# Optimization experiments

Hardware: AMD Instinct MI355X
Metric: run time of the kernel (lower is better)

## Reference

```python
import jax, jax.numpy as jnp
import numpy as np

NQ = 8           # n_qubits_q
NL = 4           # n_layers_q_circuit
NW = NQ + 1      # device wires = n_qubits + 1
DIM = 768        # input_dim == output_dim
BATCH = 4096
EPS = 1e-5

CNOT = jnp.array([[1, 0, 0, 0],
                  [0, 1, 0, 0],
                  [0, 0, 0, 1],
                  [0, 0, 1, 0]], dtype=jnp.complex64).reshape(2, 2, 2, 2)


def rx_mat(t):
    c = jnp.cos(t / 2).astype(jnp.complex64)
    s = (-1j) * jnp.sin(t / 2).astype(jnp.complex64)
    return jnp.stack([jnp.stack([c, s]), jnp.stack([s, c])])


def ry_mat(t):
    c = jnp.cos(t / 2).astype(jnp.complex64)
    s = jnp.sin(t / 2).astype(jnp.complex64)
    return jnp.stack([jnp.stack([c, -s]), jnp.stack([s, c])])


def rz_mat(t):
    e = jnp.exp(-0.5j * t.astype(jnp.complex64))
    z = jnp.zeros_like(e)
    return jnp.stack([jnp.stack([e, z]), jnp.stack([z, jnp.conj(e)])])


def apply1(state, U, w):
    # state: (2,)*NW tensor; contract gate onto wire w
    st = jnp.tensordot(U, state, axes=((1,), (w,)))
    return jnp.moveaxis(st, 0, w)


def apply2(state, G, c, t):
    # G: (2,2,2,2) gate acting on (control, target)
    st = jnp.tensordot(G, state, axes=((2, 3), (c, t)))
    return jnp.moveaxis(st, (0, 1), (c, t))


def circuit(inp, w):
    # inp: [NQ] encoded angles, w: [NL, NQ+1] circuit weights
    state = jnp.zeros((2,) * NW, jnp.complex64).at[(0,) * NW].set(1.0)
    for i in range(NQ):
        state = apply1(state, rx_mat(inp[i]), i)
        state = apply1(state, rz_mat(inp[i]), i)
    for i in range(NQ):
        state = apply1(state, rx_mat(w[0, i]), i)
        state = apply1(state, rz_mat(w[1, i]), i)
    for l in range(1, NL):
        for i in range(NQ):
            state = apply2(state, CNOT, i, (i + 1) % NQ)
            state = apply1(state, ry_mat(w[l, i]), i)
            state = apply1(state, rz_mat(w[l, i]), i)
        state = apply2(state, CNOT, NQ - 1, NQ)
        state = apply1(state, ry_mat(w[l, NQ]), NQ)
    probs = jnp.abs(state) ** 2
    z = []
    for i in range(NQ):
        other = tuple(a for a in range(NW) if a != i)
        p = probs.sum(other)          # [2]
        z.append(p[0] - p[1])         # <Z_i>
    return jnp.stack(z)               # [NQ]


def setup_inputs() -> dict:
    key = jax.random.key(0)
    ks = jax.random.split(key, 6)
    x = jax.random.normal(ks[0], (BATCH, DIM), jnp.float32)
    w_in = jax.random.normal(ks[1], (NQ, DIM), jnp.float32) * np.float32(1.0 / np.sqrt(DIM))
    b_in = jnp.zeros((NQ,), jnp.float32)
    gamma = jnp.ones((NQ,), jnp.float32)
    beta = jnp.zeros((NQ,), jnp.float32)
    q_w = jax.random.uniform(ks[2], (NL, NQ + 1), jnp.float32, 0.0, 2.0 * np.pi)
    w_out = jax.random.normal(ks[3], (DIM, NQ), jnp.float32) * np.float32(1.0 / np.sqrt(NQ))
    b_out = jnp.zeros((DIM,), jnp.float32)
    return {"x": x, "w_in": w_in, "b_in": b_in, "gamma": gamma, "beta": beta,
            "q_w": q_w, "w_out": w_out, "b_out": b_out}


def reference(x, w_in, b_in, gamma, beta, q_w, w_out, b_out):
    h = jnp.tanh(x @ w_in.T + b_in)                 # input_proj + tanh, [B, NQ]
    mu = h.mean(-1, keepdims=True)
    var = ((h - mu) ** 2).mean(-1, keepdims=True)
    hn = (h - mu) / jnp.sqrt(var + EPS) * gamma + beta   # LayerNorm
    hn = jax.lax.stop_gradient(hn)                  # torch .detach() before quantum
    qz = jax.vmap(circuit, in_axes=(0, None))(hn, q_w)   # [B, NQ] expvals
    out = qz @ w_out.T + b_out                      # output_proj
    return x + out                                   # residual (input_dim == output_dim)
```

## Files before the change

### kernel.cpp

```cpp
#include <hip/hip_runtime.h>
#include <math.h>

#define DIM   768
#define BATCH 4096
#define NQ    8
#define EPSLN 1e-5f


__device__ __forceinline__ float shflx(float v, int m) { return __shfl_xor(v, m, 64); }

template<int W>
__device__ __forceinline__ void gate_rz(float (&re)[8], float (&im)[8],
                                        float c, float s, int lane) {
  if constexpr (W < 3) {
#pragma unroll
    for (int r = 0; r < 8; ++r) {
      const float t = ((r >> W) & 1) ? s : -s;
      const float xx = re[r], yy = im[r];
      re[r] = xx * c - yy * t;
      im[r] = yy * c + xx * t;
    }
  } else {
    const float t = ((lane >> (W - 3)) & 1) ? s : -s;
#pragma unroll
    for (int r = 0; r < 8; ++r) {
      const float xx = re[r], yy = im[r];
      re[r] = xx * c - yy * t;
      im[r] = yy * c + xx * t;
    }
  }
}

template<int W>
__device__ __forceinline__ void gate_rx(float (&re)[8], float (&im)[8],
                                        float c, float s) {
  if constexpr (W < 3) {
#pragma unroll
    for (int r = 0; r < 8; ++r) {
      if (!((r >> W) & 1)) {
        const int r2 = r | (1 << W);
        const float ar = re[r], ai = im[r], br = re[r2], bi = im[r2];
        re[r]  = c * ar + s * bi;
        im[r]  = c * ai - s * br;
        re[r2] = c * br + s * ai;
        im[r2] = c * bi - s * ar;
      }
    }
  } else {
    const int mask = 1 << (W - 3);
#pragma unroll
    for (int r = 0; r < 8; ++r) {
      const float ore = shflx(re[r], mask);
      const float oim = shflx(im[r], mask);
      const float xx = re[r], yy = im[r];
      re[r] = c * xx + s * oim;
      im[r] = c * yy - s * ore;
    }
  }
}

template<int W>
__device__ __forceinline__ void gate_ry(float (&re)[8], float (&im)[8],
                                        float c, float s, int lane) {
  if constexpr (W < 3) {
#pragma unroll
    for (int r = 0; r < 8; ++r) {
      if (!((r >> W) & 1)) {
        const int r2 = r | (1 << W);
        const float ar = re[r], ai = im[r], br = re[r2], bi = im[r2];
        re[r]  = c * ar - s * br;
        im[r]  = c * ai - s * bi;
        re[r2] = s * ar + c * br;
        im[r2] = s * ai + c * bi;
      }
    }
  } else {
    const int mask = 1 << (W - 3);
    const float t = ((lane >> (W - 3)) & 1) ? s : -s;
#pragma unroll
    for (int r = 0; r < 8; ++r) {
      const float ore = shflx(re[r], mask);
      const float oim = shflx(im[r], mask);
      re[r] = c * re[r] + t * ore;
      im[r] = c * im[r] + t * oim;
    }
  }
}

template<int C, int T>
__device__ __forceinline__ void gate_cnot(float (&re)[8], float (&im)[8], int lane) {
  if constexpr (C < 3 && T < 3) {
#pragma unroll
    for (int r = 0; r < 8; ++r) {
      if (((r >> C) & 1) && !((r >> T) & 1)) {
        const int r2 = r | (1 << T);
        const float tr = re[r], ti = im[r];
        re[r] = re[r2]; im[r] = im[r2];
        re[r2] = tr;    im[r2] = ti;
      }
    }
  } else if constexpr (C < 3) {
    const int mask = 1 << (T - 3);
#pragma unroll
    for (int r = 0; r < 8; ++r) {
      if ((r >> C) & 1) {
        re[r] = shflx(re[r], mask);
        im[r] = shflx(im[r], mask);
      }
    }
  } else if constexpr (T < 3) {
    const bool cc = (lane >> (C - 3)) & 1;
#pragma unroll
    for (int r = 0; r < 8; ++r) {
      if (!((r >> T) & 1)) {
        const int r2 = r | (1 << T);
        const float ar = re[r], ai = im[r], br = re[r2], bi = im[r2];
        re[r]  = cc ? br : ar;  im[r]  = cc ? bi : ai;
        re[r2] = cc ? ar : br;  im[r2] = cc ? ai : bi;
      }
    }
  } else {
    const int mask = 1 << (T - 3);
    const bool cc = (lane >> (C - 3)) & 1;
#pragma unroll
    for (int r = 0; r < 8; ++r) {
      const float ore = shflx(re[r], mask);
      const float oim = shflx(im[r], mask);
      re[r] = cc ? ore : re[r];
      im[r] = cc ? oim : im[r];
    }
  }
}

__global__ void precompute_trig(const float* __restrict__ qw, float* __restrict__ cs) {
  const int i = threadIdx.x;
  if (i < 36) {
    float s, c;
    sincosf(0.5f * qw[i], &s, &c);
    cs[2 * i]     = c;
    cs[2 * i + 1] = s;
  }
}

__global__ __launch_bounds__(256, 4)
void quantum_fused(const float* __restrict__ x,
                   const float* __restrict__ w_in,
                   const float* __restrict__ b_in,
                   const float* __restrict__ gamma,
                   const float* __restrict__ beta,
                   const float* __restrict__ w_out,
                   const float* __restrict__ b_out,
                   const float* __restrict__ cs,
                   float* __restrict__ out) {
  const int lane = threadIdx.x & 63;
  const int wv   = threadIdx.x >> 6;
  const int row  = blockIdx.x * 4 + wv;

  const float* xrow = x + (size_t)row * DIM;
  const float4* xv  = (const float4*)xrow;

  float4 xr[3];
#pragma unroll
  for (int k = 0; k < 3; ++k) xr[k] = xv[lane + 64 * k];

  float h[8];
#pragma unroll
  for (int q = 0; q < 8; ++q) {
    const float4* wq = (const float4*)(w_in + q * DIM);
    float acc = 0.f;
#pragma unroll
    for (int k = 0; k < 3; ++k) {
      const float4 w4 = wq[lane + 64 * k];
      acc += xr[k].x * w4.x + xr[k].y * w4.y + xr[k].z * w4.z + xr[k].w * w4.w;
    }
    h[q] = acc;
  }
#pragma unroll
  for (int m = 1; m < 64; m <<= 1) {
#pragma unroll
    for (int q = 0; q < 8; ++q) h[q] += shflx(h[q], m);
  }

#pragma unroll
  for (int q = 0; q < 8; ++q) h[q] = tanhf(h[q] + b_in[q]);
  float mu = 0.f;
#pragma unroll
  for (int q = 0; q < 8; ++q) mu += h[q];
  mu *= 0.125f;
  float var = 0.f;
#pragma unroll
  for (int q = 0; q < 8; ++q) { const float d = h[q] - mu; var += d * d; }
  var *= 0.125f;
  const float inv = 1.0f / sqrtf(var + EPSLN);
  float ang[8];
#pragma unroll
  for (int q = 0; q < 8; ++q)
    ang[q] = (h[q] - mu) * inv * gamma[q] + beta[q];

  float re[8], im[8];
#pragma unroll
  for (int r = 0; r < 8; ++r) { re[r] = 0.f; im[r] = 0.f; }
  re[0] = (lane == 0) ? 1.f : 0.f;

#define ENC_I(i) { float s_, c_; sincosf(0.5f * ang[i], &s_, &c_);            \
                   gate_rx<i>(re, im, c_, s_);                                 \
                   gate_rz<i>(re, im, c_, s_, lane); }
  ENC_I(0) ENC_I(1) ENC_I(2) ENC_I(3) ENC_I(4) ENC_I(5) ENC_I(6) ENC_I(7)
#undef ENC_I

#define L0_I(i) { gate_rx<i>(re, im, cs[2*(i)], cs[2*(i)+1]);                  \
                  gate_rz<i>(re, im, cs[2*(9+(i))], cs[2*(9+(i))+1], lane); }
  L0_I(0) L0_I(1) L0_I(2) L0_I(3) L0_I(4) L0_I(5) L0_I(6) L0_I(7)
#undef L0_I

#define LSTEP(l, i, j) { gate_cnot<i, j>(re, im, lane);                        \
                         const float c_ = cs[2*((l)*9+(i))];                   \
                         const float s_ = cs[2*((l)*9+(i))+1];                 \
                         gate_ry<i>(re, im, c_, s_, lane);                     \
                         gate_rz<i>(re, im, c_, s_, lane); }
#define LAYER(l)                                                               \
  LSTEP(l,0,1) LSTEP(l,1,2) LSTEP(l,2,3) LSTEP(l,3,4)                          \
  LSTEP(l,4,5) LSTEP(l,5,6) LSTEP(l,6,7) LSTEP(l,7,0)                          \
  { gate_cnot<7, 8>(re, im, lane);                                             \
    gate_ry<8>(re, im, cs[2*((l)*9+8)], cs[2*((l)*9+8)+1], lane); }
  LAYER(1) LAYER(2) LAYER(3)
#undef LAYER
#undef LSTEP

  float p[8];
#pragma unroll
  for (int r = 0; r < 8; ++r) p[r] = re[r] * re[r] + im[r] * im[r];
  float ptot = 0.f;
#pragma unroll
  for (int r = 0; r < 8; ++r) ptot += p[r];
  float z[8];
#pragma unroll
  for (int i = 0; i < 3; ++i) {
    float acc = 0.f;
#pragma unroll
    for (int r = 0; r < 8; ++r) acc += ((r >> i) & 1) ? -p[r] : p[r];
    z[i] = acc;
  }
#pragma unroll
  for (int i = 3; i < 8; ++i)
    z[i] = ((lane >> (i - 3)) & 1) ? -ptot : ptot;
#pragma unroll
  for (int m = 1; m < 64; m <<= 1) {
#pragma unroll
    for (int i = 0; i < 8; ++i) z[i] += shflx(z[i], m);
  }

  float* orow = out + (size_t)row * DIM;
  float4* ov = (float4*)orow;
  const float4* bv = (const float4*)b_out;
#pragma unroll
  for (int k = 0; k < 3; ++k) {
    const int j4 = lane + 64 * k;
    const float4 b4 = bv[j4];
    const float4* wo = (const float4*)(w_out + (size_t)j4 * 32);
    const float4 r0a = wo[0], r0b = wo[1];
    const float4 r1a = wo[2], r1b = wo[3];
    const float4 r2a = wo[4], r2b = wo[5];
    const float4 r3a = wo[6], r3b = wo[7];
    float4 o;
    o.x = xr[k].x + b4.x + z[0]*r0a.x + z[1]*r0a.y + z[2]*r0a.z + z[3]*r0a.w
                        + z[4]*r0b.x + z[5]*r0b.y + z[6]*r0b.z + z[7]*r0b.w;
    o.y = xr[k].y + b4.y + z[0]*r1a.x + z[1]*r1a.y + z[2]*r1a.z + z[3]*r1a.w
                        + z[4]*r1b.x + z[5]*r1b.y + z[6]*r1b.z + z[7]*r1b.w;
    o.z = xr[k].z + b4.z + z[0]*r2a.x + z[1]*r2a.y + z[2]*r2a.z + z[3]*r2a.w
                        + z[4]*r2b.x + z[5]*r2b.y + z[6]*r2b.z + z[7]*r2b.w;
    o.w = xr[k].w + b4.w + z[0]*r3a.x + z[1]*r3a.y + z[2]*r3a.z + z[3]*r3a.w
                        + z[4]*r3b.x + z[5]*r3b.y + z[6]*r3b.z + z[7]*r3b.w;
    ov[j4] = o;
  }
}

extern "C" void kernel_launch(void* const* d_in, const int* in_sizes, int n_in,
                              void* d_out, int out_size, void* d_ws, size_t ws_size,
                              hipStream_t stream) {
  const float* x     = (const float*)d_in[0];
  const float* w_in  = (const float*)d_in[1];
  const float* b_in  = (const float*)d_in[2];
  const float* gamma = (const float*)d_in[3];
  const float* beta  = (const float*)d_in[4];
  const float* q_w   = (const float*)d_in[5];
  const float* w_out = (const float*)d_in[6];
  const float* b_out = (const float*)d_in[7];
  float* outp = (float*)d_out;
  float* cs   = (float*)d_ws;

  hipLaunchKernelGGL(precompute_trig, dim3(1), dim3(64), 0, stream, q_w, cs);
  hipLaunchKernelGGL(quantum_fused, dim3(BATCH / 4), dim3(256), 0, stream,
                     x, w_in, b_in, gamma, beta, w_out, b_out, cs, outp);
}
```

Measured before the change: 118.4 us.

## Process two batch rows per wavefront to amortize weight loads and shuffles

Each wavefront now simulates two circuits at once, holding 16 complex amplitudes per lane, and the grid shrinks to BATCH/8 blocks. The w_in, w_out and gate-parameter loads and the per-gate control logic are shared between the two rows, and batching the shuffles into arrays gives more instruction-level parallelism to hide cross-lane latency. In exchange, register pressure roughly doubles (launch bounds lowered to 2 waves) and fewer waves are resident to hide memory latency.

```diff
diff --git a/kernel.cpp b/kernel.cpp
--- a/kernel.cpp
+++ b/kernel.cpp
@@ -10,20 +10,25 @@
 __device__ __forceinline__ float shflx(float v, int m) { return __shfl_xor(v, m, 64); }
 
 template<int W>
-__device__ __forceinline__ void gate_rz(float (&re)[8], float (&im)[8],
-                                        float c, float s, int lane) {
+__device__ __forceinline__ void gate_rz(float (&re)[16], float (&im)[16],
+                                        float c0, float s0, float c1, float s1,
+                                        int lane) {
   if constexpr (W < 3) {
 #pragma unroll
-    for (int r = 0; r < 8; ++r) {
-      const float t = ((r >> W) & 1) ? s : -s;
+    for (int r = 0; r < 16; ++r) {
+      const float c = (r < 8) ? c0 : c1;
+      const float t = (((r >> W) & 1) ? 1.f : -1.f) * ((r < 8) ? s0 : s1);
       const float xx = re[r], yy = im[r];
       re[r] = xx * c - yy * t;
       im[r] = yy * c + xx * t;
     }
   } else {
-    const float t = ((lane >> (W - 3)) & 1) ? s : -s;
-#pragma unroll
-    for (int r = 0; r < 8; ++r) {
+    const float sgn = ((lane >> (W - 3)) & 1) ? 1.f : -1.f;
+    const float t0 = sgn * s0, t1 = sgn * s1;
+#pragma unroll
+    for (int r = 0; r < 16; ++r) {
+      const float c = (r < 8) ? c0 : c1;
+      const float t = (r < 8) ? t0 : t1;
       const float xx = re[r], yy = im[r];
       re[r] = xx * c - yy * t;
       im[r] = yy * c + xx * t;
@@ -32,13 +37,15 @@
 }
 
 template<int W>
-__device__ __forceinline__ void gate_rx(float (&re)[8], float (&im)[8],
-                                        float c, float s) {
+__device__ __forceinline__ void gate_rx(float (&re)[16], float (&im)[16],
+                                        float c0, float s0, float c1, float s1) {
   if constexpr (W < 3) {
 #pragma unroll
-    for (int r = 0; r < 8; ++r) {
+    for (int r = 0; r < 16; ++r) {
       if (!((r >> W) & 1)) {
         const int r2 = r | (1 << W);
+        const float c = (r < 8) ? c0 : c1;
+        const float s = (r < 8) ? s0 : s1;
         const float ar = re[r], ai = im[r], br = re[r2], bi = im[r2];
         re[r]  = c * ar + s * bi;
         im[r]  = c * ai - s * br;
@@ -48,25 +55,31 @@
     }
   } else {
     const int mask = 1 << (W - 3);
-#pragma unroll
-    for (int r = 0; r < 8; ++r) {
-      const float ore = shflx(re[r], mask);
-      const float oim = shflx(im[r], mask);
+    float ore[16], oim[16];
+#pragma unroll
+    for (int r = 0; r < 16; ++r) { ore[r] = shflx(re[r], mask); oim[r] = shflx(im[r], mask); }
+#pragma unroll
+    for (int r = 0; r < 16; ++r) {
+      const float c = (r < 8) ? c0 : c1;
+      const float s = (r < 8) ? s0 : s1;
       const float xx = re[r], yy = im[r];
-      re[r] = c * xx + s * oim;
-      im[r] = c * yy - s * ore;
+      re[r] = c * xx + s * oim[r];
+      im[r] = c * yy - s * ore[r];
     }
   }
 }
 
 template<int W>
-__device__ __forceinline__ void gate_ry(float (&re)[8], float (&im)[8],
-                                        float c, float s, int lane) {
+__device__ __forceinline__ void gate_ry(float (&re)[16], float (&im)[16],
+                                        float c0, float s0, float c1, float s1,
+                                        int lane) {
   if constexpr (W < 3) {
 #pragma unroll
-    for (int r = 0; r < 8; ++r) {
+    for (int r = 0; r < 16; ++r) {
       if (!((r >> W) & 1)) {
         const int r2 = r | (1 << W);
+        const float c = (r < 8) ? c0 : c1;
+        const float s = (r < 8) ? s0 : s1;
         const float ar = re[r], ai = im[r], br = re[r2], bi = im[r2];
         re[r]  = c * ar - s * br;
         im[r]  = c * ai - s * bi;
@@ -76,22 +89,26 @@
     }
   } else {
     const int mask = 1 << (W - 3);
-    const float t = ((lane >> (W - 3)) & 1) ? s : -s;
-#pragma unroll
-    for (int r = 0; r < 8; ++r) {
-      const float ore = shflx(re[r], mask);
-      const float oim = shflx(im[r], mask);
-      re[r] = c * re[r] + t * ore;
-      im[r] = c * im[r] + t * oim;
+    const float sgn = ((lane >> (W - 3)) & 1) ? 1.f : -1.f;
+    const float t0 = sgn * s0, t1 = sgn * s1;
+    float ore[16], oim[16];
+#pragma unroll
+    for (int r = 0; r < 16; ++r) { ore[r] = shflx(re[r], mask); oim[r] = shflx(im[r], mask); }
+#pragma unroll
+    for (int r = 0; r < 16; ++r) {
+      const float c = (r < 8) ? c0 : c1;
+      const float t = (r < 8) ? t0 : t1;
+      re[r] = c * re[r] + t * ore[r];
+      im[r] = c * im[r] + t * oim[r];
     }
   }
 }
 
 template<int C, int T>
-__device__ __forceinline__ void gate_cnot(float (&re)[8], float (&im)[8], int lane) {
+__device__ __forceinline__ void gate_cnot(float (&re)[16], float (&im)[16], int lane) {
   if constexpr (C < 3 && T < 3) {
 #pragma unroll
-    for (int r = 0; r < 8; ++r) {
+    for (int r = 0; r < 16; ++r) {
       if (((r >> C) & 1) && !((r >> T) & 1)) {
         const int r2 = r | (1 << T);
         const float tr = re[r], ti = im[r];
@@ -102,7 +119,7 @@
   } else if constexpr (C < 3) {
     const int mask = 1 << (T - 3);
 #pragma unroll
-    for (int r = 0; r < 8; ++r) {
+    for (int r = 0; r < 16; ++r) {
       if ((r >> C) & 1) {
         re[r] = shflx(re[r], mask);
         im[r] = shflx(im[r], mask);
@@ -111,7 +128,7 @@
   } else if constexpr (T < 3) {
     const bool cc = (lane >> (C - 3)) & 1;
 #pragma unroll
-    for (int r = 0; r < 8; ++r) {
+    for (int r = 0; r < 16; ++r) {
       if (!((r >> T) & 1)) {
         const int r2 = r | (1 << T);
         const float ar = re[r], ai = im[r], br = re[r2], bi = im[r2];
@@ -122,12 +139,13 @@
   } else {
     const int mask = 1 << (T - 3);
     const bool cc = (lane >> (C - 3)) & 1;
-#pragma unroll
-    for (int r = 0; r < 8; ++r) {
-      const float ore = shflx(re[r], mask);
-      const float oim = shflx(im[r], mask);
-      re[r] = cc ? ore : re[r];
-      im[r] = cc ? oim : im[r];
+    float ore[16], oim[16];
+#pragma unroll
+    for (int r = 0; r < 16; ++r) { ore[r] = shflx(re[r], mask); oim[r] = shflx(im[r], mask); }
+#pragma unroll
+    for (int r = 0; r < 16; ++r) {
+      re[r] = cc ? ore[r] : re[r];
+      im[r] = cc ? oim[r] : im[r];
     }
   }
 }
@@ -142,7 +160,7 @@
   }
 }
 
-__global__ __launch_bounds__(256, 4)
+__global__ __launch_bounds__(256, 2)
 void quantum_fused(const float* __restrict__ x,
                    const float* __restrict__ w_in,
                    const float* __restrict__ b_in,
@@ -154,124 +172,148 @@
                    float* __restrict__ out) {
   const int lane = threadIdx.x & 63;
   const int wv   = threadIdx.x >> 6;
-  const int row  = blockIdx.x * 4 + wv;
-
-  const float* xrow = x + (size_t)row * DIM;
-  const float4* xv  = (const float4*)xrow;
-
-  float4 xr[3];
-#pragma unroll
-  for (int k = 0; k < 3; ++k) xr[k] = xv[lane + 64 * k];
-
-  float h[8];
+  const int rowA = blockIdx.x * 8 + wv * 2;
+  const int rowB = rowA + 1;
+
+  const float4* xvA = (const float4*)(x + (size_t)rowA * DIM);
+  const float4* xvB = (const float4*)(x + (size_t)rowB * DIM);
+
+  float4 xrA[3], xrB[3];
+#pragma unroll
+  for (int k = 0; k < 3; ++k) { xrA[k] = xvA[lane + 64 * k]; xrB[k] = xvB[lane + 64 * k]; }
+
+  float h[16];
 #pragma unroll
   for (int q = 0; q < 8; ++q) {
     const float4* wq = (const float4*)(w_in + q * DIM);
-    float acc = 0.f;
+    float aA = 0.f, aB = 0.f;
 #pragma unroll
     for (int k = 0; k < 3; ++k) {
       const float4 w4 = wq[lane + 64 * k];
-      acc += xr[k].x * w4.x + xr[k].y * w4.y + xr[k].z * w4.z + xr[k].w * w4.w;
-    }
-    h[q] = acc;
+      aA += xrA[k].x * w4.x + xrA[k].y * w4.y + xrA[k].z * w4.z + xrA[k].w * w4.w;
+      aB += xrB[k].x * w4.x + xrB[k].y * w4.y + xrB[k].z * w4.z + xrB[k].w * w4.w;
+    }
+    h[q] = aA; h[8 + q] = aB;
   }
 #pragma unroll
   for (int m = 1; m < 64; m <<= 1) {
 #pragma unroll
-    for (int q = 0; q < 8; ++q) h[q] += shflx(h[q], m);
-  }
-
-#pragma unroll
-  for (int q = 0; q < 8; ++q) h[q] = tanhf(h[q] + b_in[q]);
-  float mu = 0.f;
-#pragma unroll
-  for (int q = 0; q < 8; ++q) mu += h[q];
-  mu *= 0.125f;
-  float var = 0.f;
-#pragma unroll
-  for (int q = 0; q < 8; ++q) { const float d = h[q] - mu; var += d * d; }
-  var *= 0.125f;
-  const float inv = 1.0f / sqrtf(var + EPSLN);
-  float ang[8];
-#pragma unroll
-  for (int q = 0; q < 8; ++q)
-    ang[q] = (h[q] - mu) * inv * gamma[q] + beta[q];
-
-  float re[8], im[8];
-#pragma unroll
-  for (int r = 0; r < 8; ++r) { re[r] = 0.f; im[r] = 0.f; }
+    for (int q = 0; q < 16; ++q) h[q] += shflx(h[q], m);
+  }
+
+  float ang[16];
+#pragma unroll
+  for (int rowi = 0; rowi < 2; ++rowi) {
+    const int o = rowi * 8;
+#pragma unroll
+    for (int q = 0; q < 8; ++q) h[o + q] = tanhf(h[o + q] + b_in[q]);
+    float mu = 0.f;
+#pragma unroll
+    for (int q = 0; q < 8; ++q) mu += h[o + q];
+    mu *= 0.125f;
+    float var = 0.f;
+#pragma unroll
+    for (int q = 0; q < 8; ++q) { const float d = h[o + q] - mu; var += d * d; }
+    var *= 0.125f;
+    const float inv = 1.0f / sqrtf(var + EPSLN);
+#pragma unroll
+    for (int q = 0; q < 8; ++q)
+      ang[o + q] = (h[o + q] - mu) * inv * gamma[q] + beta[q];
+  }
+
+  float re[16], im[16];
+#pragma unroll
+  for (int r = 0; r < 16; ++r) { re[r] = 0.f; im[r] = 0.f; }
   re[0] = (lane == 0) ? 1.f : 0.f;
-
-#define ENC_I(i) { float s_, c_; sincosf(0.5f * ang[i], &s_, &c_);            \
-                   gate_rx<i>(re, im, c_, s_);                                 \
-                   gate_rz<i>(re, im, c_, s_, lane); }
+  re[8] = (lane == 0) ? 1.f : 0.f;
+
+#define ENC_I(i) { float sA, cA, sB, cB;                                       \
+                   sincosf(0.5f * ang[i], &sA, &cA);                           \
+                   sincosf(0.5f * ang[8 + i], &sB, &cB);                       \
+                   gate_rx<i>(re, im, cA, sA, cB, sB);                         \
+                   gate_rz<i>(re, im, cA, sA, cB, sB, lane); }
   ENC_I(0) ENC_I(1) ENC_I(2) ENC_I(3) ENC_I(4) ENC_I(5) ENC_I(6) ENC_I(7)
 #undef ENC_I
 
-#define L0_I(i) { gate_rx<i>(re, im, cs[2*(i)], cs[2*(i)+1]);                  \
-                  gate_rz<i>(re, im, cs[2*(9+(i))], cs[2*(9+(i))+1], lane); }
+#define L0_I(i) { const float c0 = cs[2*(i)],     s0 = cs[2*(i)+1];            \
+                  const float c1 = cs[2*(9+(i))], s1 = cs[2*(9+(i))+1];        \
+                  gate_rx<i>(re, im, c0, s0, c0, s0);                          \
+                  gate_rz<i>(re, im, c1, s1, c1, s1, lane); }
   L0_I(0) L0_I(1) L0_I(2) L0_I(3) L0_I(4) L0_I(5) L0_I(6) L0_I(7)
 #undef L0_I
 
 #define LSTEP(l, i, j) { gate_cnot<i, j>(re, im, lane);                        \
                          const float c_ = cs[2*((l)*9+(i))];                   \
                          const float s_ = cs[2*((l)*9+(i))+1];                 \
-                         gate_ry<i>(re, im, c_, s_, lane);                     \
-                         gate_rz<i>(re, im, c_, s_, lane); }
+                         gate_ry<i>(re, im, c_, s_, c_, s_, lane);             \
+                         gate_rz<i>(re, im, c_, s_, c_, s_, lane); }
 #define LAYER(l)                                                               \
   LSTEP(l,0,1) LSTEP(l,1,2) LSTEP(l,2,3) LSTEP(l,3,4)                          \
   LSTEP(l,4,5) LSTEP(l,5,6) LSTEP(l,6,7) LSTEP(l,7,0)                          \
   { gate_cnot<7, 8>(re, im, lane);                                             \
-    gate_ry<8>(re, im, cs[2*((l)*9+8)], cs[2*((l)*9+8)+1], lane); }
+    gate_ry<8>(re, im, cs[2*((l)*9+8)], cs[2*((l)*9+8)+1],                     \
+                        cs[2*((l)*9+8)], cs[2*((l)*9+8)+1], lane); }
   LAYER(1) LAYER(2) LAYER(3)
 #undef LAYER
 #undef LSTEP
 
-  float p[8];
-#pragma unroll
-  for (int r = 0; r < 8; ++r) p[r] = re[r] * re[r] + im[r] * im[r];
-  float ptot = 0.f;
-#pragma unroll
-  for (int r = 0; r < 8; ++r) ptot += p[r];
-  float z[8];
+  float p[16];
+#pragma unroll
+  for (int r = 0; r < 16; ++r) p[r] = re[r] * re[r] + im[r] * im[r];
+  float ptotA = 0.f, ptotB = 0.f;
+#pragma unroll
+  for (int r = 0; r < 8; ++r) { ptotA += p[r]; ptotB += p[8 + r]; }
+  float z[16];
 #pragma unroll
   for (int i = 0; i < 3; ++i) {
-    float acc = 0.f;
-#pragma unroll
-    for (int r = 0; r < 8; ++r) acc += ((r >> i) & 1) ? -p[r] : p[r];
-    z[i] = acc;
-  }
-#pragma unroll
-  for (int i = 3; i < 8; ++i)
-    z[i] = ((lane >> (i - 3)) & 1) ? -ptot : ptot;
+    float aA = 0.f, aB = 0.f;
+#pragma unroll
+    for (int r = 0; r < 8; ++r) {
+      const float sg = ((r >> i) & 1) ? -1.f : 1.f;
+      aA += sg * p[r];
+      aB += sg * p[8 + r];
+    }
+    z[i] = aA; z[8 + i] = aB;
+  }
+#pragma unroll
+  for (int i = 3; i < 8; ++i) {
+    const float sg = ((lane >> (i - 3)) & 1) ? -1.f : 1.f;
+    z[i] = sg * ptotA;
+    z[8 + i] = sg * ptotB;
+  }
 #pragma unroll
   for (int m = 1; m < 64; m <<= 1) {
 #pragma unroll
-    for (int i = 0; i < 8; ++i) z[i] += shflx(z[i], m);
-  }
-
-  float* orow = out + (size_t)row * DIM;
-  float4* ov = (float4*)orow;
-  const float4* bv = (const float4*)b_out;
-#pragma unroll
-  for (int k = 0; k < 3; ++k) {
-    const int j4 = lane + 64 * k;
-    const float4 b4 = bv[j4];
-    const float4* wo = (const float4*)(w_out + (size_t)j4 * 32);
-    const float4 r0a = wo[0], r0b = wo[1];
-    const float4 r1a = wo[2], r1b = wo[3];
-    const float4 r2a = wo[4], r2b = wo[5];
-    const float4 r3a = wo[6], r3b = wo[7];
-    float4 o;
-    o.x = xr[k].x + b4.x + z[0]*r0a.x + z[1]*r0a.y + z[2]*r0a.z + z[3]*r0a.w
-                        + z[4]*r0b.x + z[5]*r0b.y + z[6]*r0b.z + z[7]*r0b.w;
-    o.y = xr[k].y + b4.y + z[0]*r1a.x + z[1]*r1a.y + z[2]*r1a.z + z[3]*r1a.w
-                        + z[4]*r1b.x + z[5]*r1b.y + z[6]*r1b.z + z[7]*r1b.w;
-    o.z = xr[k].z + b4.z + z[0]*r2a.x + z[1]*r2a.y + z[2]*r2a.z + z[3]*r2a.w
-                        + z[4]*r2b.x + z[5]*r2b.y + z[6]*r2b.z + z[7]*r2b.w;
-    o.w = xr[k].w + b4.w + z[0]*r3a.x + z[1]*r3a.y + z[2]*r3a.z + z[3]*r3a.w
-                        + z[4]*r3b.x + z[5]*r3b.y + z[6]*r3b.z + z[7]*r3b.w;
-    ov[j4] = o;
+    for (int i = 0; i < 16; ++i) z[i] += shflx(z[i], m);
+  }
+
+#pragma unroll
+  for (int rowi = 0; rowi < 2; ++rowi) {
+    const int row = rowi ? rowB : rowA;
+    const float4* xr = rowi ? xrB : xrA;
+    const float* zz = z + rowi * 8;
+    float4* ov = (float4*)(out + (size_t)row * DIM);
+    const float4* bv = (const float4*)b_out;
+#pragma unroll
+    for (int k = 0; k < 3; ++k) {
+      const int j4 = lane + 64 * k;
+      const float4 b4 = bv[j4];
+      const float4* wo = (const float4*)(w_out + (size_t)j4 * 32);
+      const float4 r0a = wo[0], r0b = wo[1];
+      const float4 r1a = wo[2], r1b = wo[3];
+      const float4 r2a = wo[4], r2b = wo[5];
+      const float4 r3a = wo[6], r3b = wo[7];
+      float4 o;
+      o.x = xr[k].x + b4.x + zz[0]*r0a.x + zz[1]*r0a.y + zz[2]*r0a.z + zz[3]*r0a.w
+                          + zz[4]*r0b.x + zz[5]*r0b.y + zz[6]*r0b.z + zz[7]*r0b.w;
+      o.y = xr[k].y + b4.y + zz[0]*r1a.x + zz[1]*r1a.y + zz[2]*r1a.z + zz[3]*r1a.w
+                          + zz[4]*r1b.x + zz[5]*r1b.y + zz[6]*r1b.z + zz[7]*r1b.w;
+      o.z = xr[k].z + b4.z + zz[0]*r2a.x + zz[1]*r2a.y + zz[2]*r2a.z + zz[3]*r2a.w
+                          + zz[4]*r2b.x + zz[5]*r2b.y + zz[6]*r2b.z + zz[7]*r2b.w;
+      o.w = xr[k].w + b4.w + zz[0]*r3a.x + zz[1]*r3a.y + zz[2]*r3a.z + zz[3]*r3a.w
+                          + zz[4]*r3b.x + zz[5]*r3b.y + zz[6]*r3b.z + zz[7]*r3b.w;
+      ov[j4] = o;
+    }
   }
 }
 
@@ -290,6 +332,6 @@
   float* cs   = (float*)d_ws;
 
   hipLaunchKernelGGL(precompute_trig, dim3(1), dim3(64), 0, stream, q_w, cs);
-  hipLaunchKernelGGL(quantum_fused, dim3(BATCH / 4), dim3(256), 0, stream,
+  hipLaunchKernelGGL(quantum_fused, dim3(BATCH / 8), dim3(256), 0, stream,
                      x, w_in, b_in, gamma, beta, w_out, b_out, cs, outp);
 }
```

Result: slower. 127.7 us (+7.8%).

## Build product-state analytically, remap qubit lanes, use DPP/swizzle cross-lane ops

Applied to the files above, without the earlier changes.

The encoding and first-layer rotations act on separate qubits, so the state after them is a product state. It is now built directly as a tensor product of per-qubit 2-vectors instead of applying 32 gates with shuffles. Qubit-to-lane-bit assignments are permuted so the most frequent cross-lane partners map to cheap DPP or ds_swizzle patterns, and permlane32_swap is used for xor 32 where the builtin exists. Reductions use the same fast cross-lane primitives. The risks are the faster __sincosf losing precision and errors in the bit mapping.

```diff
diff --git a/kernel.cpp b/kernel.cpp
--- a/kernel.cpp
+++ b/kernel.cpp
@@ -3,11 +3,58 @@
 
 #define DIM   768
 #define BATCH 4096
-#define NQ    8
 #define EPSLN 1e-5f
 
 
-__device__ __forceinline__ float shflx(float v, int m) { return __shfl_xor(v, m, 64); }
+__host__ __device__ constexpr int bitof(int W) {
+  return W == 3 ? 4 : W == 4 ? 0 : W == 5 ? 1 : W == 6 ? 3 : W == 7 ? 5 : 2;
+}
+
+template<int CTRL>
+__device__ __forceinline__ float dppf(float v) {
+  return __int_as_float(__builtin_amdgcn_update_dpp(
+      0, __float_as_int(v), CTRL, 0xF, 0xF, false));
+}
+template<int OFF>
+__device__ __forceinline__ float swzf(float v) {
+  return __int_as_float(__builtin_amdgcn_ds_swizzle(__float_as_int(v), OFF));
+}
+__device__ __forceinline__ float xor32f(float v, int lane) {
+#if __has_builtin(__builtin_amdgcn_permlane32_swap)
+  typedef int i2_t __attribute__((ext_vector_type(2)));
+  i2_t r = __builtin_amdgcn_permlane32_swap(__float_as_int(v), __float_as_int(v),
+                                            false, false);
+  return __int_as_float((lane >= 32) ? r.x : r.y);
+#else
+  return __shfl_xor(v, 32, 64);
+#endif
+}
+
+template<int M>
+__device__ __forceinline__ float lxor(float v, int lane) {
+  if constexpr (M == 1)       return dppf<0xB1>(v);
+  else if constexpr (M == 2)  return dppf<0x4E>(v);
+  else if constexpr (M == 4)  return swzf<0x101F>(v);
+  else if constexpr (M == 8)  return dppf<0x128>(v);
+  else if constexpr (M == 16) return swzf<0x401F>(v);
+  else                        return xor32f(v, lane);
+}
+
+template<int N>
+__device__ __forceinline__ void allred(float (&v)[N], int lane) {
+#pragma unroll
+  for (int q = 0; q < N; ++q) v[q] += lxor<1>(v[q], lane);
+#pragma unroll
+  for (int q = 0; q < N; ++q) v[q] += lxor<2>(v[q], lane);
+#pragma unroll
+  for (int q = 0; q < N; ++q) v[q] += lxor<4>(v[q], lane);
+#pragma unroll
+  for (int q = 0; q < N; ++q) v[q] += lxor<8>(v[q], lane);
+#pragma unroll
+  for (int q = 0; q < N; ++q) v[q] += lxor<16>(v[q], lane);
+#pragma unroll
+  for (int q = 0; q < N; ++q) v[q] += lxor<32>(v[q], lane);
+}
 
 template<int W>
 __device__ __forceinline__ void gate_rz(float (&re)[8], float (&im)[8],
@@ -21,40 +68,12 @@
       im[r] = yy * c + xx * t;
     }
   } else {
-    const float t = ((lane >> (W - 3)) & 1) ? s : -s;
+    const float t = ((lane >> bitof(W)) & 1) ? s : -s;
 #pragma unroll
     for (int r = 0; r < 8; ++r) {
       const float xx = re[r], yy = im[r];
       re[r] = xx * c - yy * t;
       im[r] = yy * c + xx * t;
-    }
-  }
-}
-
-template<int W>
-__device__ __forceinline__ void gate_rx(float (&re)[8], float (&im)[8],
-                                        float c, float s) {
-  if constexpr (W < 3) {
-#pragma unroll
-    for (int r = 0; r < 8; ++r) {
-      if (!((r >> W) & 1)) {
-        const int r2 = r | (1 << W);
-        const float ar = re[r], ai = im[r], br = re[r2], bi = im[r2];
-        re[r]  = c * ar + s * bi;
-        im[r]  = c * ai - s * br;
-        re[r2] = c * br + s * ai;
-        im[r2] = c * bi - s * ar;
-      }
-    }
-  } else {
-    const int mask = 1 << (W - 3);
-#pragma unroll
-    for (int r = 0; r < 8; ++r) {
-      const float ore = shflx(re[r], mask);
-      const float oim = shflx(im[r], mask);
-      const float xx = re[r], yy = im[r];
-      re[r] = c * xx + s * oim;
-      im[r] = c * yy - s * ore;
     }
   }
 }
@@ -75,12 +94,12 @@
       }
     }
   } else {
-    const int mask = 1 << (W - 3);
-    const float t = ((lane >> (W - 3)) & 1) ? s : -s;
-#pragma unroll
-    for (int r = 0; r < 8; ++r) {
-      const float ore = shflx(re[r], mask);
-      const float oim = shflx(im[r], mask);
+    constexpr int M = 1 << bitof(W);
+    const float t = ((lane >> bitof(W)) & 1) ? s : -s;
+#pragma unroll
+    for (int r = 0; r < 8; ++r) {
+      const float ore = lxor<M>(re[r], lane);
+      const float oim = lxor<M>(im[r], lane);
       re[r] = c * re[r] + t * ore;
       im[r] = c * im[r] + t * oim;
     }
@@ -100,16 +119,16 @@
       }
     }
   } else if constexpr (C < 3) {
-    const int mask = 1 << (T - 3);
+    constexpr int M = 1 << bitof(T);
 #pragma unroll
     for (int r = 0; r < 8; ++r) {
       if ((r >> C) & 1) {
-        re[r] = shflx(re[r], mask);
-        im[r] = shflx(im[r], mask);
+        re[r] = lxor<M>(re[r], lane);
+        im[r] = lxor<M>(im[r], lane);
       }
     }
   } else if constexpr (T < 3) {
-    const bool cc = (lane >> (C - 3)) & 1;
+    const bool cc = (lane >> bitof(C)) & 1;
 #pragma unroll
     for (int r = 0; r < 8; ++r) {
       if (!((r >> T) & 1)) {
@@ -120,16 +139,23 @@
       }
     }
   } else {
-    const int mask = 1 << (T - 3);
-    const bool cc = (lane >> (C - 3)) & 1;
-#pragma unroll
-    for (int r = 0; r < 8; ++r) {
-      const float ore = shflx(re[r], mask);
-      const float oim = shflx(im[r], mask);
-      re[r] = cc ? ore : re[r];
-      im[r] = cc ? oim : im[r];
-    }
-  }
+    constexpr int M = 1 << bitof(T);
+    const bool cc = (lane >> bitof(C)) & 1;
+#pragma unroll
+    for (int r = 0; r < 8; ++r) {
+      const float orr = lxor<M>(re[r], lane);
+      const float oii = lxor<M>(im[r], lane);
+      re[r] = cc ? orr : re[r];
+      im[r] = cc ? oii : im[r];
+    }
+  }
+}
+
+__device__ __forceinline__ void cmul(float& dr, float& di,
+                                     float ar, float ai, float br, float bi) {
+  const float rr = ar * br - ai * bi;
+  const float ii = ar * bi + ai * br;
+  dr = rr; di = ii;
 }
 
 __global__ void precompute_trig(const float* __restrict__ qw, float* __restrict__ cs) {
@@ -156,9 +182,7 @@
   const int wv   = threadIdx.x >> 6;
   const int row  = blockIdx.x * 4 + wv;
 
-  const float* xrow = x + (size_t)row * DIM;
-  const float4* xv  = (const float4*)xrow;
-
+  const float4* xv = (const float4*)(x + (size_t)row * DIM);
   float4 xr[3];
 #pragma unroll
   for (int k = 0; k < 3; ++k) xr[k] = xv[lane + 64 * k];
@@ -175,11 +199,7 @@
     }
     h[q] = acc;
   }
-#pragma unroll
-  for (int m = 1; m < 64; m <<= 1) {
-#pragma unroll
-    for (int q = 0; q < 8; ++q) h[q] += shflx(h[q], m);
-  }
+  allred(h, lane);
 
 #pragma unroll
   for (int q = 0; q < 8; ++q) h[q] = tanhf(h[q] + b_in[q]);
@@ -197,21 +217,56 @@
   for (int q = 0; q < 8; ++q)
     ang[q] = (h[q] - mu) * inv * gamma[q] + beta[q];
 
+  float f0r[8], f0i[8], f1r[8], f1i[8];
+#pragma unroll
+  for (int i = 0; i < 8; ++i) {
+    float sa, ca;
+    __sincosf(0.5f * ang[i], &sa, &ca);
+    const float p0r = ca * ca, p0i = -ca * sa;
+    const float p1r = sa * sa, p1i = -sa * ca;
+    const float c0 = cs[2 * i],        s0 = cs[2 * i + 1];
+    const float cz = cs[2 * (9 + i)],  sz = cs[2 * (9 + i) + 1];
+    const float q0r = c0 * p0r + s0 * p1i, q0i = c0 * p0i - s0 * p1r;
+    const float q1r = s0 * p0i + c0 * p1r, q1i = -s0 * p0r + c0 * p1i;
+    f0r[i] = cz * q0r + sz * q0i;  f0i[i] = cz * q0i - sz * q0r;
+    f1r[i] = cz * q1r - sz * q1i;  f1i[i] = cz * q1i + sz * q1r;
+  }
+
+  float tr[8], ti[8];
+  tr[0] = f0r[0]; ti[0] = f0i[0];
+  tr[1] = f1r[0]; ti[1] = f1i[0];
+#pragma unroll
+  for (int b = 0; b < 2; ++b) {
+    cmul(tr[2 + b], ti[2 + b], tr[b], ti[b], f1r[1], f1i[1]);
+    cmul(tr[b],     ti[b],     tr[b], ti[b], f0r[1], f0i[1]);
+  }
+#pragma unroll
+  for (int b = 0; b < 4; ++b) {
+    cmul(tr[4 + b], ti[4 + b], tr[b], ti[b], f1r[2], f1i[2]);
+    cmul(tr[b],     ti[b],     tr[b], ti[b], f0r[2], f0i[2]);
+  }
+
+  float Lr, Li;
+  {
+    const bool b3 = (lane >> bitof(3)) & 1;
+    Lr = b3 ? f1r[3] : f0r[3];
+    Li = b3 ? f1i[3] : f0i[3];
+#pragma unroll
+    for (int i = 4; i < 8; ++i) {
+      const bool b = (lane >> bitof(i)) & 1;
+      const float gr = b ? f1r[i] : f0r[i];
+      const float gi = b ? f1i[i] : f0i[i];
+      cmul(Lr, Li, Lr, Li, gr, gi);
+    }
+    if ((lane >> bitof(8)) & 1) { Lr = 0.f; Li = 0.f; }
+  }
+
   float re[8], im[8];
 #pragma unroll
-  for (int r = 0; r < 8; ++r) { re[r] = 0.f; im[r] = 0.f; }
-  re[0] = (lane == 0) ? 1.f : 0.f;
-
-#define ENC_I(i) { float s_, c_; sincosf(0.5f * ang[i], &s_, &c_);            \
-                   gate_rx<i>(re, im, c_, s_);                                 \
-                   gate_rz<i>(re, im, c_, s_, lane); }
-  ENC_I(0) ENC_I(1) ENC_I(2) ENC_I(3) ENC_I(4) ENC_I(5) ENC_I(6) ENC_I(7)
-#undef ENC_I
-
-#define L0_I(i) { gate_rx<i>(re, im, cs[2*(i)], cs[2*(i)+1]);                  \
-                  gate_rz<i>(re, im, cs[2*(9+(i))], cs[2*(9+(i))+1], lane); }
-  L0_I(0) L0_I(1) L0_I(2) L0_I(3) L0_I(4) L0_I(5) L0_I(6) L0_I(7)
-#undef L0_I
+  for (int r = 0; r < 8; ++r) {
+    re[r] = tr[r] * Lr - ti[r] * Li;
+    im[r] = tr[r] * Li + ti[r] * Lr;
+  }
 
 #define LSTEP(l, i, j) { gate_cnot<i, j>(re, im, lane);                        \
                          const float c_ = cs[2*((l)*9+(i))];                   \
@@ -243,12 +298,8 @@
   }
 #pragma unroll
   for (int i = 3; i < 8; ++i)
-    z[i] = ((lane >> (i - 3)) & 1) ? -ptot : ptot;
-#pragma unroll
-  for (int m = 1; m < 64; m <<= 1) {
-#pragma unroll
-    for (int i = 0; i < 8; ++i) z[i] += shflx(z[i], m);
-  }
+    z[i] = ((lane >> bitof(i)) & 1) ? -ptot : ptot;
+  allred(z, lane);
 
   float* orow = out + (size_t)row * DIM;
   float4* ov = (float4*)orow;
```

Result: faster. 106.0 us (-10.5%).

## Analytic product-state encoding, qubit-to-lane remap, DPP shuffles and packed FMA

Applied to the files above, without the earlier changes.

Replaces the gate-by-gate encoding and first layer with an analytic product-state construction, since before any CNOT each qubit evolves independently. Qubits are remapped onto register and lane bits so most cross-lane exchanges can use DPP or ds_swizzle instead of generic shuffles. The complex state is stored as float2 so packed FMA can be used. The per-qubit Z reductions are replaced by a Walsh-Hadamard butterfly followed by readlane. These changes target ALU and cross-lane exchange cost, at the price of more intricate bit-mapping logic where an error would give wrong results.

```diff
diff --git a/kernel.cpp b/kernel.cpp
--- a/kernel.cpp
+++ b/kernel.cpp
@@ -3,133 +3,151 @@
 
 #define DIM   768
 #define BATCH 4096
-#define NQ    8
 #define EPSLN 1e-5f
 
 
-__device__ __forceinline__ float shflx(float v, int m) { return __shfl_xor(v, m, 64); }
-
+typedef float v2f __attribute__((ext_vector_type(2)));
+
+__device__ __forceinline__ v2f pkfma(v2f a, v2f b, v2f c) {
+  return __builtin_elementwise_fma(a, b, c);
+}
+
+template<int CTRL>
+__device__ __forceinline__ float dppf(float v) {
+  return __int_as_float(__builtin_amdgcn_update_dpp(
+      0, __float_as_int(v), CTRL, 0xF, 0xF, false));
+}
+template<int OFF>
+__device__ __forceinline__ float swzf(float v) {
+  return __int_as_float(__builtin_amdgcn_ds_swizzle(__float_as_int(v), OFF));
+}
+
+template<int M>
+__device__ __forceinline__ float lxor(float v, int bpx) {
+  if constexpr (M == 1)       return dppf<0xB1>(v);
+  else if constexpr (M == 2)  return dppf<0x4E>(v);
+  else if constexpr (M == 4)  return swzf<0x101F>(v);
+  else if constexpr (M == 8)  return dppf<0x128>(v);
+  else if constexpr (M == 16) return swzf<0x401F>(v);
+  else return __int_as_float(__builtin_amdgcn_ds_bpermute(bpx, __float_as_int(v)));
+}
+template<int M>
+__device__ __forceinline__ v2f lxor2(v2f v, int bpx) {
+  v2f r; r.x = lxor<M>(v.x, bpx); r.y = lxor<M>(v.y, bpx); return r;
+}
+
+__host__ __device__ constexpr int wbit(int w) {
+  return w == 2 ? 2 : w == 3 ? 0 : w == 4 ? 1 : w == 5 ? 3 : w == 6 ? 4 : 5;
+}
+__host__ __device__ constexpr int wmask(int w) { return 1 << wbit(w); }
+
+__device__ __forceinline__ float rdlane(float v, int l) {
+  return __int_as_float(__builtin_amdgcn_readlane(__float_as_int(v), l));
+}
+__device__ __forceinline__ float rdfirst(float v) {
+  return __int_as_float(__builtin_amdgcn_readfirstlane(__float_as_int(v)));
+}
+
+__device__ __forceinline__ v2f cmul(v2f a, v2f b) {
+  v2f r;
+  r.x = fmaf(a.x, b.x, -(a.y * b.y));
+  r.y = fmaf(a.x, b.y,   a.y * b.x);
+  return r;
+}
+
+template<int B>
+__device__ __forceinline__ void rz_local(v2f (&a)[8], float c, float s) {
+  const v2f cc = {c, c};
+  const v2f t1 = {-s, s};
+  const v2f t0 = {s, -s};
+#pragma unroll
+  for (int r = 0; r < 8; ++r) {
+    const v2f tt = ((r >> B) & 1) ? t1 : t0;
+    v2f sw; sw.x = a[r].y; sw.y = a[r].x;
+    a[r] = pkfma(tt, sw, cc * a[r]);
+  }
+}
 template<int W>
-__device__ __forceinline__ void gate_rz(float (&re)[8], float (&im)[8],
-                                        float c, float s, int lane) {
-  if constexpr (W < 3) {
-#pragma unroll
-    for (int r = 0; r < 8; ++r) {
-      const float t = ((r >> W) & 1) ? s : -s;
-      const float xx = re[r], yy = im[r];
-      re[r] = xx * c - yy * t;
-      im[r] = yy * c + xx * t;
+__device__ __forceinline__ void rz_lane(v2f (&a)[8], float c, float s, bool bit) {
+  const float t = bit ? s : -s;
+  const v2f cc = {c, c}, tv = {-t, t};
+#pragma unroll
+  for (int r = 0; r < 8; ++r) {
+    v2f sw; sw.x = a[r].y; sw.y = a[r].x;
+    a[r] = pkfma(tv, sw, cc * a[r]);
+  }
+}
+template<int B>
+__device__ __forceinline__ void ry_local(v2f (&a)[8], float c, float s) {
+  const v2f cc = {c, c}, sv = {s, s}, ns = {-s, -s};
+#pragma unroll
+  for (int r = 0; r < 8; ++r) {
+    if (!((r >> B) & 1)) {
+      const int r2 = r | (1 << B);
+      const v2f lo = a[r], hi = a[r2];
+      a[r]  = pkfma(ns, hi, cc * lo);
+      a[r2] = pkfma(sv, lo, cc * hi);
     }
-  } else {
-    const float t = ((lane >> (W - 3)) & 1) ? s : -s;
-#pragma unroll
-    for (int r = 0; r < 8; ++r) {
-      const float xx = re[r], yy = im[r];
-      re[r] = xx * c - yy * t;
-      im[r] = yy * c + xx * t;
+  }
+}
+template<int W>
+__device__ __forceinline__ void ry_lane(v2f (&a)[8], float c, float s, bool bit, int bpx) {
+  constexpr int M = wmask(W);
+  const float t = bit ? s : -s;
+  const v2f cc = {c, c}, tv = {t, t};
+#pragma unroll
+  for (int r = 0; r < 8; ++r) {
+    const v2f o = lxor2<M>(a[r], bpx);
+    a[r] = pkfma(tv, o, cc * a[r]);
+  }
+}
+__device__ __forceinline__ void cnot01(v2f (&a)[8]) {
+  v2f t = a[1]; a[1] = a[3]; a[3] = t;
+  t = a[5]; a[5] = a[7]; a[7] = t;
+}
+__device__ __forceinline__ void cnot12(v2f (&a)[8], int bpx) {
+  a[2] = lxor2<4>(a[2], bpx);
+  a[3] = lxor2<4>(a[3], bpx);
+  a[6] = lxor2<4>(a[6], bpx);
+  a[7] = lxor2<4>(a[7], bpx);
+}
+template<int T>
+__device__ __forceinline__ void cnot_ll(v2f (&a)[8], bool cc, int bpx) {
+  constexpr int M = wmask(T);
+#pragma unroll
+  for (int r = 0; r < 8; ++r) {
+    const v2f o = lxor2<M>(a[r], bpx);
+    a[r].x = cc ? o.x : a[r].x;
+    a[r].y = cc ? o.y : a[r].y;
+  }
+}
+template<int B>
+__device__ __forceinline__ void cnot_lt(v2f (&a)[8], bool cc) {
+#pragma unroll
+  for (int r = 0; r < 8; ++r) {
+    if (!((r >> B) & 1)) {
+      const int r2 = r | (1 << B);
+      const v2f lo = a[r], hi = a[r2];
+      a[r].x  = cc ? hi.x : lo.x;  a[r].y  = cc ? hi.y : lo.y;
+      a[r2].x = cc ? lo.x : hi.x;  a[r2].y = cc ? lo.y : hi.y;
     }
   }
 }
 
-template<int W>
-__device__ __forceinline__ void gate_rx(float (&re)[8], float (&im)[8],
-                                        float c, float s) {
-  if constexpr (W < 3) {
-#pragma unroll
-    for (int r = 0; r < 8; ++r) {
-      if (!((r >> W) & 1)) {
-        const int r2 = r | (1 << W);
-        const float ar = re[r], ai = im[r], br = re[r2], bi = im[r2];
-        re[r]  = c * ar + s * bi;
-        im[r]  = c * ai - s * br;
-        re[r2] = c * br + s * ai;
-        im[r2] = c * bi - s * ar;
-      }
-    }
-  } else {
-    const int mask = 1 << (W - 3);
-#pragma unroll
-    for (int r = 0; r < 8; ++r) {
-      const float ore = shflx(re[r], mask);
-      const float oim = shflx(im[r], mask);
-      const float xx = re[r], yy = im[r];
-      re[r] = c * xx + s * oim;
-      im[r] = c * yy - s * ore;
-    }
-  }
-}
-
-template<int W>
-__device__ __forceinline__ void gate_ry(float (&re)[8], float (&im)[8],
-                                        float c, float s, int lane) {
-  if constexpr (W < 3) {
-#pragma unroll
-    for (int r = 0; r < 8; ++r) {
-      if (!((r >> W) & 1)) {
-        const int r2 = r | (1 << W);
-        const float ar = re[r], ai = im[r], br = re[r2], bi = im[r2];
-        re[r]  = c * ar - s * br;
-        im[r]  = c * ai - s * bi;
-        re[r2] = s * ar + c * br;
-        im[r2] = s * ai + c * bi;
-      }
-    }
-  } else {
-    const int mask = 1 << (W - 3);
-    const float t = ((lane >> (W - 3)) & 1) ? s : -s;
-#pragma unroll
-    for (int r = 0; r < 8; ++r) {
-      const float ore = shflx(re[r], mask);
-      const float oim = shflx(im[r], mask);
-      re[r] = c * re[r] + t * ore;
-      im[r] = c * im[r] + t * oim;
-    }
-  }
-}
-
-template<int C, int T>
-__device__ __forceinline__ void gate_cnot(float (&re)[8], float (&im)[8], int lane) {
-  if constexpr (C < 3 && T < 3) {
-#pragma unroll
-    for (int r = 0; r < 8; ++r) {
-      if (((r >> C) & 1) && !((r >> T) & 1)) {
-        const int r2 = r | (1 << T);
-        const float tr = re[r], ti = im[r];
-        re[r] = re[r2]; im[r] = im[r2];
-        re[r2] = tr;    im[r2] = ti;
-      }
-    }
-  } else if constexpr (C < 3) {
-    const int mask = 1 << (T - 3);
-#pragma unroll
-    for (int r = 0; r < 8; ++r) {
-      if ((r >> C) & 1) {
-        re[r] = shflx(re[r], mask);
-        im[r] = shflx(im[r], mask);
-      }
-    }
-  } else if constexpr (T < 3) {
-    const bool cc = (lane >> (C - 3)) & 1;
-#pragma unroll
-    for (int r = 0; r < 8; ++r) {
-      if (!((r >> T) & 1)) {
-        const int r2 = r | (1 << T);
-        const float ar = re[r], ai = im[r], br = re[r2], bi = im[r2];
-        re[r]  = cc ? br : ar;  im[r]  = cc ? bi : ai;
-        re[r2] = cc ? ar : br;  im[r2] = cc ? ai : bi;
-      }
-    }
-  } else {
-    const int mask = 1 << (T - 3);
-    const bool cc = (lane >> (C - 3)) & 1;
-#pragma unroll
-    for (int r = 0; r < 8; ++r) {
-      const float ore = shflx(re[r], mask);
-      const float oim = shflx(im[r], mask);
-      re[r] = cc ? ore : re[r];
-      im[r] = cc ? oim : im[r];
-    }
-  }
+template<int N>
+__device__ __forceinline__ void allred(float (&v)[N], int bpx) {
+#pragma unroll
+  for (int q = 0; q < N; ++q) v[q] += lxor<1>(v[q], bpx);
+#pragma unroll
+  for (int q = 0; q < N; ++q) v[q] += lxor<2>(v[q], bpx);
+#pragma unroll
+  for (int q = 0; q < N; ++q) v[q] += lxor<4>(v[q], bpx);
+#pragma unroll
+  for (int q = 0; q < N; ++q) v[q] += lxor<8>(v[q], bpx);
+#pragma unroll
+  for (int q = 0; q < N; ++q) v[q] += lxor<16>(v[q], bpx);
+#pragma unroll
+  for (int q = 0; q < N; ++q) v[q] += lxor<32>(v[q], bpx);
 }
 
 __global__ void precompute_trig(const float* __restrict__ qw, float* __restrict__ cs) {
@@ -155,10 +173,16 @@
   const int lane = threadIdx.x & 63;
   const int wv   = threadIdx.x >> 6;
   const int row  = blockIdx.x * 4 + wv;
-
-  const float* xrow = x + (size_t)row * DIM;
-  const float4* xv  = (const float4*)xrow;
-
+  const int bpx  = ((lane ^ 32) << 2);
+
+  const bool bw2 = (lane >> 2) & 1;
+  const bool bw3 = (lane >> 0) & 1;
+  const bool bw4 = (lane >> 1) & 1;
+  const bool bw5 = (lane >> 3) & 1;
+  const bool bw6 = (lane >> 4) & 1;
+  const bool bw7 = (lane >> 5) & 1;
+
+  const float4* xv = (const float4*)(x + (size_t)row * DIM);
   float4 xr[3];
 #pragma unroll
   for (int k = 0; k < 3; ++k) xr[k] = xv[lane + 64 * k];
@@ -167,19 +191,20 @@
 #pragma unroll
   for (int q = 0; q < 8; ++q) {
     const float4* wq = (const float4*)(w_in + q * DIM);
-    float acc = 0.f;
+    v2f acc = {0.f, 0.f};
 #pragma unroll
     for (int k = 0; k < 3; ++k) {
       const float4 w4 = wq[lane + 64 * k];
-      acc += xr[k].x * w4.x + xr[k].y * w4.y + xr[k].z * w4.z + xr[k].w * w4.w;
+      v2f xa; xa.x = xr[k].x; xa.y = xr[k].y;
+      v2f xb; xb.x = xr[k].z; xb.y = xr[k].w;
+      v2f wa; wa.x = w4.x; wa.y = w4.y;
+      v2f wb; wb.x = w4.z; wb.y = w4.w;
+      acc = pkfma(xa, wa, acc);
+      acc = pkfma(xb, wb, acc);
     }
-    h[q] = acc;
-  }
-#pragma unroll
-  for (int m = 1; m < 64; m <<= 1) {
-#pragma unroll
-    for (int q = 0; q < 8; ++q) h[q] += shflx(h[q], m);
-  }
+    h[q] = acc.x + acc.y;
+  }
+  allred(h, bpx);
 
 #pragma unroll
   for (int q = 0; q < 8; ++q) h[q] = tanhf(h[q] + b_in[q]);
@@ -197,58 +222,83 @@
   for (int q = 0; q < 8; ++q)
     ang[q] = (h[q] - mu) * inv * gamma[q] + beta[q];
 
-  float re[8], im[8];
-#pragma unroll
-  for (int r = 0; r < 8; ++r) { re[r] = 0.f; im[r] = 0.f; }
-  re[0] = (lane == 0) ? 1.f : 0.f;
-
-#define ENC_I(i) { float s_, c_; sincosf(0.5f * ang[i], &s_, &c_);            \
-                   gate_rx<i>(re, im, c_, s_);                                 \
-                   gate_rz<i>(re, im, c_, s_, lane); }
-  ENC_I(0) ENC_I(1) ENC_I(2) ENC_I(3) ENC_I(4) ENC_I(5) ENC_I(6) ENC_I(7)
-#undef ENC_I
-
-#define L0_I(i) { gate_rx<i>(re, im, cs[2*(i)], cs[2*(i)+1]);                  \
-                  gate_rz<i>(re, im, cs[2*(9+(i))], cs[2*(9+(i))+1], lane); }
-  L0_I(0) L0_I(1) L0_I(2) L0_I(3) L0_I(4) L0_I(5) L0_I(6) L0_I(7)
-#undef L0_I
-
-#define LSTEP(l, i, j) { gate_cnot<i, j>(re, im, lane);                        \
-                         const float c_ = cs[2*((l)*9+(i))];                   \
-                         const float s_ = cs[2*((l)*9+(i))+1];                 \
-                         gate_ry<i>(re, im, c_, s_, lane);                     \
-                         gate_rz<i>(re, im, c_, s_, lane); }
-#define LAYER(l)                                                               \
-  LSTEP(l,0,1) LSTEP(l,1,2) LSTEP(l,2,3) LSTEP(l,3,4)                          \
-  LSTEP(l,4,5) LSTEP(l,5,6) LSTEP(l,6,7) LSTEP(l,7,0)                          \
-  { gate_cnot<7, 8>(re, im, lane);                                             \
-    gate_ry<8>(re, im, cs[2*((l)*9+8)], cs[2*((l)*9+8)+1], lane); }
+  v2f f0[8], f1[8];
+#pragma unroll
+  for (int i = 0; i < 8; ++i) {
+    float sa, ca;
+    __sincosf(0.5f * ang[i], &sa, &ca);
+    const float p0r = ca * ca, p0i = -ca * sa;
+    const float p1r = sa * sa, p1i = -sa * ca;
+    const float c0 = cs[2 * i],       s0 = cs[2 * i + 1];
+    const float cz = cs[2 * (9 + i)], sz = cs[2 * (9 + i) + 1];
+    const float q0r = c0 * p0r + s0 * p1i, q0i = c0 * p0i - s0 * p1r;
+    const float q1r = s0 * p0i + c0 * p1r, q1i = -s0 * p0r + c0 * p1i;
+    f0[i].x = cz * q0r + sz * q0i;  f0[i].y = cz * q0i - sz * q0r;
+    f1[i].x = cz * q1r - sz * q1i;  f1[i].y = cz * q1i + sz * q1r;
+  }
+
+  v2f t01[4];
+  t01[0] = cmul(f0[0], f0[1]);
+  t01[1] = cmul(f1[0], f0[1]);
+  t01[2] = cmul(f0[0], f1[1]);
+  t01[3] = cmul(f1[0], f1[1]);
+  v2f L = bw2 ? f1[2] : f0[2];
+  L = cmul(L, bw3 ? f1[3] : f0[3]);
+  L = cmul(L, bw4 ? f1[4] : f0[4]);
+  L = cmul(L, bw5 ? f1[5] : f0[5]);
+  L = cmul(L, bw6 ? f1[6] : f0[6]);
+  L = cmul(L, bw7 ? f1[7] : f0[7]);
+
+  v2f a[8];
+#pragma unroll
+  for (int r = 0; r < 4; ++r) a[r] = cmul(t01[r], L);
+#pragma unroll
+  for (int r = 4; r < 8; ++r) { a[r].x = 0.f; a[r].y = 0.f; }
+
+#define G(l, i) cs[2 * ((l) * 9 + (i))], cs[2 * ((l) * 9 + (i)) + 1]
+#define LAYER(l)                                                                 \
+  cnot01(a);               ry_local<0>(a, G(l,0)); rz_local<0>(a, G(l,0));       \
+  cnot12(a, bpx);          ry_local<1>(a, G(l,1)); rz_local<1>(a, G(l,1));       \
+  cnot_ll<3>(a, bw2, bpx); ry_lane<2>(a, G(l,2), bw2, bpx); rz_lane<2>(a, G(l,2), bw2); \
+  cnot_ll<4>(a, bw3, bpx); ry_lane<3>(a, G(l,3), bw3, bpx); rz_lane<3>(a, G(l,3), bw3); \
+  cnot_ll<5>(a, bw4, bpx); ry_lane<4>(a, G(l,4), bw4, bpx); rz_lane<4>(a, G(l,4), bw4); \
+  cnot_ll<6>(a, bw5, bpx); ry_lane<5>(a, G(l,5), bw5, bpx); rz_lane<5>(a, G(l,5), bw5); \
+  cnot_ll<7>(a, bw6, bpx); ry_lane<6>(a, G(l,6), bw6, bpx); rz_lane<6>(a, G(l,6), bw6); \
+  cnot_lt<0>(a, bw7);      ry_lane<7>(a, G(l,7), bw7, bpx); rz_lane<7>(a, G(l,7), bw7); \
+  cnot_lt<2>(a, bw7);      ry_local<2>(a, G(l,8));
   LAYER(1) LAYER(2) LAYER(3)
 #undef LAYER
-#undef LSTEP
+#undef G
 
   float p[8];
 #pragma unroll
-  for (int r = 0; r < 8; ++r) p[r] = re[r] * re[r] + im[r] * im[r];
-  float ptot = 0.f;
-#pragma unroll
-  for (int r = 0; r < 8; ++r) ptot += p[r];
+  for (int r = 0; r < 8; ++r) p[r] = fmaf(a[r].x, a[r].x, a[r].y * a[r].y);
+  const float S = ((p[0] + p[1]) + (p[2] + p[3])) + ((p[4] + p[5]) + (p[6] + p[7]));
+  float zz[2];
+  zz[0] = ((p[0] - p[1]) + (p[2] - p[3])) + ((p[4] - p[5]) + (p[6] - p[7]));
+  zz[1] = ((p[0] + p[1]) - (p[2] + p[3])) + ((p[4] + p[5]) - (p[6] + p[7]));
+  allred(zz, bpx);
+
+  float sg[6];
+#pragma unroll
+  for (int b = 0; b < 6; ++b) sg[b] = ((lane >> b) & 1) ? -1.f : 1.f;
+  float W = S, t_;
+  t_ = lxor<1>(W, bpx);  W = fmaf(sg[0], W, t_);
+  t_ = lxor<2>(W, bpx);  W = fmaf(sg[1], W, t_);
+  t_ = lxor<4>(W, bpx);  W = fmaf(sg[2], W, t_);
+  t_ = lxor<8>(W, bpx);  W = fmaf(sg[3], W, t_);
+  t_ = lxor<16>(W, bpx); W = fmaf(sg[4], W, t_);
+  t_ = lxor<32>(W, bpx); W = fmaf(sg[5], W, t_);
+
   float z[8];
-#pragma unroll
-  for (int i = 0; i < 3; ++i) {
-    float acc = 0.f;
-#pragma unroll
-    for (int r = 0; r < 8; ++r) acc += ((r >> i) & 1) ? -p[r] : p[r];
-    z[i] = acc;
-  }
-#pragma unroll
-  for (int i = 3; i < 8; ++i)
-    z[i] = ((lane >> (i - 3)) & 1) ? -ptot : ptot;
-#pragma unroll
-  for (int m = 1; m < 64; m <<= 1) {
-#pragma unroll
-    for (int i = 0; i < 8; ++i) z[i] += shflx(z[i], m);
-  }
+  z[0] = rdfirst(zz[0]);
+  z[1] = rdfirst(zz[1]);
+  z[2] = rdlane(W, 4);
+  z[3] = rdlane(W, 1);
+  z[4] = rdlane(W, 2);
+  z[5] = rdlane(W, 8);
+  z[6] = rdlane(W, 16);
+  z[7] = rdlane(W, 32);
 
   float* orow = out + (size_t)row * DIM;
   float4* ov = (float4*)orow;
```

Measured after the change: 102.1 us. -13.8%, faster.
